# Kernel optimization log

Measured on AMD Instinct MI355X. Metric: run time of the kernel, lower is better.

Reference implementation:

```python
import jax, jax.numpy as jnp
from jax import lax
import numpy as np

INPUT = 80
H1 = 100
H2 = 50


def _lstm_layer(x, Wih, Whh, bih, bhh):
    """PyTorch-semantics single-layer LSTM, batch_first.
    x: [B,T,I]; Wih: [4H,I]; Whh: [4H,H]; biases: [4H]. Gate order: i,f,g,o.
    Returns full hidden sequence [B,T,H]."""
    B, T, _ = x.shape
    H = Whh.shape[1]
    # precompute input projections for all timesteps (one big GEMM)
    pre = jnp.einsum('bti,gi->tbg', x, Wih) + (bih + bhh)  # [T,B,4H]

    def step(carry, p):
        h, c = carry
        gates = p + h @ Whh.T  # [B,4H]
        i, f, g, o = jnp.split(gates, 4, axis=-1)
        i = jax.nn.sigmoid(i)
        f = jax.nn.sigmoid(f)
        g = jnp.tanh(g)
        o = jax.nn.sigmoid(o)
        c = f * c + i * g
        h = o * jnp.tanh(c)
        return (h, c), h

    h0 = jnp.zeros((B, H), x.dtype)
    (_, _), hs = lax.scan(step, (h0, h0), pre)  # hs: [T,B,H]
    return jnp.transpose(hs, (1, 0, 2))  # [B,T,H]


def setup_inputs() -> dict:
    key = jax.random.key(0)
    ks = jax.random.split(key, 9)
    B, T = 1024, 512
    s1 = 1.0 / np.sqrt(H1)
    s2 = 1.0 / np.sqrt(H2)
    return {
        'x': jax.random.normal(ks[0], (B, T, INPUT), dtype=jnp.float32),
        'Wih1': jax.random.uniform(ks[1], (4 * H1, INPUT), jnp.float32, -s1, s1),
        'Whh1': jax.random.uniform(ks[2], (4 * H1, H1), jnp.float32, -s1, s1),
        'bih1': jax.random.uniform(ks[3], (4 * H1,), jnp.float32, -s1, s1),
        'bhh1': jax.random.uniform(ks[4], (4 * H1,), jnp.float32, -s1, s1),
        'Wih2': jax.random.uniform(ks[5], (4 * H2, H1), jnp.float32, -s2, s2),
        'Whh2': jax.random.uniform(ks[6], (4 * H2, H2), jnp.float32, -s2, s2),
        'bih2': jax.random.uniform(ks[7], (4 * H2,), jnp.float32, -s2, s2),
        'bhh2': jax.random.uniform(ks[8], (4 * H2,), jnp.float32, -s2, s2),
    }


def reference(x, Wih1, Whh1, bih1, bhh1, Wih2, Whh2, bih2, bhh2):
    # Dropout layers are identity in eval mode.
    h1 = _lstm_layer(x, Wih1, Whh1, bih1, bhh1)   # [B,T,100]
    h2 = _lstm_layer(h1, Wih2, Whh2, bih2, bhh2)  # [B,T,50]
    return h2[:, -1, :]                            # [B,50]
```

## Files before the change

kernel.cpp:

```cpp
#include <hip/hip_runtime.h>

#define BT 1024
#define TT 512

__device__ __forceinline__ float sig_(float x) { return 1.f / (1.f + __expf(-x)); }
__device__ __forceinline__ float th_(float x)  { return 1.f - 2.f / (1.f + __expf(2.f * x)); }

template <int KS, int KPAD, int KH, int N, bool XMODE>
__device__ __forceinline__ void gp_stage(
    const float* __restrict__ A, const float* __restrict__ W,
    float (&As)[128][KPAD], float (&Bs)[KPAD][128],
    int tid, int n0, int by, int t0, int k0)
{
    constexpr int NQH = KH / 4;
#pragma unroll
    for (int ii = tid; ii < 128 * NQH; ii += 256) {
        int r = ii / NQH, q = ii % NQH;
        const float* src;
        if (XMODE) {
            int b  = (by & 7) * 128 + r;
            int tl = by >> 3;
            src = A + ((size_t)b * TT + (t0 + tl)) * KS;
        } else {
            src = A + (size_t)(by * 128 + r) * KS;
        }
        *(float4*)&As[r][q * 4] = *(const float4*)(src + k0 + q * 4);
    }
#pragma unroll
    for (int ii = tid; ii < 128 * NQH; ii += 256) {
        int n = ii & 127, kq = ii >> 7;
        float4 v = make_float4(0.f, 0.f, 0.f, 0.f);
        if (n0 + n < N) v = *(const float4*)(W + (size_t)(n0 + n) * KS + k0 + kq * 4);
        Bs[kq * 4 + 0][n] = v.x; Bs[kq * 4 + 1][n] = v.y;
        Bs[kq * 4 + 2][n] = v.z; Bs[kq * 4 + 3][n] = v.w;
    }
}

template <int KPAD, int KH>
__device__ __forceinline__ void gp_compute(
    const float (&As)[128][KPAD], const float (&Bs)[KPAD][128],
    float (&acc)[8][8], int tx, int ty)
{
    for (int kk = 0; kk < KH; kk += 4) {
        float4 bv[4][2];
#pragma unroll
        for (int r = 0; r < 4; r++) {
            bv[r][0] = *(const float4*)&Bs[kk + r][tx * 8];
            bv[r][1] = *(const float4*)&Bs[kk + r][tx * 8 + 4];
        }
#pragma unroll
        for (int i = 0; i < 8; i++) {
            float4 av = *(const float4*)&As[ty + 16 * i][kk];
#pragma unroll
            for (int s = 0; s < 2; s++) {
                acc[i][s*4+0] = fmaf(av.x, bv[0][s].x, acc[i][s*4+0]);
                acc[i][s*4+0] = fmaf(av.y, bv[1][s].x, acc[i][s*4+0]);
                acc[i][s*4+0] = fmaf(av.z, bv[2][s].x, acc[i][s*4+0]);
                acc[i][s*4+0] = fmaf(av.w, bv[3][s].x, acc[i][s*4+0]);
                acc[i][s*4+1] = fmaf(av.x, bv[0][s].y, acc[i][s*4+1]);
                acc[i][s*4+1] = fmaf(av.y, bv[1][s].y, acc[i][s*4+1]);
                acc[i][s*4+1] = fmaf(av.z, bv[2][s].y, acc[i][s*4+1]);
                acc[i][s*4+1] = fmaf(av.w, bv[3][s].y, acc[i][s*4+1]);
                acc[i][s*4+2] = fmaf(av.x, bv[0][s].z, acc[i][s*4+2]);
                acc[i][s*4+2] = fmaf(av.y, bv[1][s].z, acc[i][s*4+2]);
                acc[i][s*4+2] = fmaf(av.z, bv[2][s].z, acc[i][s*4+2]);
                acc[i][s*4+2] = fmaf(av.w, bv[3][s].z, acc[i][s*4+2]);
                acc[i][s*4+3] = fmaf(av.x, bv[0][s].w, acc[i][s*4+3]);
                acc[i][s*4+3] = fmaf(av.y, bv[1][s].w, acc[i][s*4+3]);
                acc[i][s*4+3] = fmaf(av.z, bv[2][s].w, acc[i][s*4+3]);
                acc[i][s*4+3] = fmaf(av.w, bv[3][s].w, acc[i][s*4+3]);
            }
        }
    }
}

template <int KS, int KPAD, int KH0, int N, bool XMODE>
__global__ __launch_bounds__(256, 3) void gemm_pre(
    const float* __restrict__ A, const float* __restrict__ W,
    const float* __restrict__ bih, const float* __restrict__ bhh,
    float* __restrict__ out, int t0)
{
    constexpr int KH1 = KS - KH0;
    __shared__ __align__(16) float As[128][KPAD];
    __shared__ __align__(16) float Bs[KPAD][128];
    const int tid = threadIdx.x;
    const int n0 = blockIdx.x * 128;
    const int by = blockIdx.y;
    const int Rbase = by * 128;
    const int tx = tid & 15, ty = tid >> 4;

    float acc[8][8];
#pragma unroll
    for (int i = 0; i < 8; i++)
#pragma unroll
        for (int j = 0; j < 8; j++) acc[i][j] = 0.f;

    gp_stage<KS, KPAD, KH0, N, XMODE>(A, W, As, Bs, tid, n0, by, t0, 0);
    __syncthreads();
    gp_compute<KPAD, KH0>(As, Bs, acc, tx, ty);
    __syncthreads();
    gp_stage<KS, KPAD, KH1, N, XMODE>(A, W, As, Bs, tid, n0, by, t0, KH0);
    __syncthreads();
    gp_compute<KPAD, KH1>(As, Bs, acc, tx, ty);

#pragma unroll
    for (int s = 0; s < 2; s++) {
        int n = n0 + tx * 8 + s * 4;
        if (n < N) {
            float4 bias;
            bias.x = bih[n] + bhh[n];         bias.y = bih[n + 1] + bhh[n + 1];
            bias.z = bih[n + 2] + bhh[n + 2]; bias.w = bih[n + 3] + bhh[n + 3];
#pragma unroll
            for (int i = 0; i < 8; i++) {
                size_t R = (size_t)Rbase + ty + 16 * i;
                float4 o;
                o.x = acc[i][s*4+0] + bias.x; o.y = acc[i][s*4+1] + bias.y;
                o.z = acc[i][s*4+2] + bias.z; o.w = acc[i][s*4+3] + bias.w;
                *(float4*)(out + R * N + n) = o;
            }
        }
    }
}

struct __align__(16) R1S {
    float hs[2][100];
    float pres[2][800];
    float gbuf[5 * 4 * 2 * 100];
};
struct __align__(16) R2S {
    float hs[2][50];
    float pres[2][400];
    float gbuf[5 * 4 * 2 * 50];
};
union __align__(16) FS { R1S r1; R2S r2[2]; };

__device__ __forceinline__ void rec1_body(
    R1S& s, int tid, int b0,
    const float* __restrict__ pre, const float* __restrict__ Whh,
    float* __restrict__ hseq, float* __restrict__ cst, int Tc, int first)
{
    const bool comp = tid < 500;
    const int j  = tid % 100;
    const int kq = tid / 100;

    float4 w[4][5];
    if (comp) {
#pragma unroll
        for (int g = 0; g < 4; g++) {
            const float4* W4 = (const float4*)(Whh + (size_t)(g * 100 + j) * 100);
#pragma unroll
            for (int q = 0; q < 5; q++) w[g][q] = W4[kq * 5 + q];
        }
    }

    const bool upd = tid < 200;
    const int ub = tid / 100, uj = tid % 100;
    float c = 0.f;
    if (upd) {
        float h = 0.f;
        if (!first) {
            h = hseq[((size_t)(Tc - 1) * BT + b0 + ub) * 100 + uj];
            c = cst[(size_t)(b0 + ub) * 100 + uj];
        }
        s.hs[ub][uj] = h;
        ((float4*)s.pres[0])[tid] = ((const float4*)(pre + (size_t)b0 * 400))[tid];
    }
    __syncthreads();

    int cur = 0;
    for (int t = 0; t < Tc; t++) {
        int tn = (t + 1 < Tc) ? (t + 1) : t;
        float4 pf0;
        if (upd)
            pf0 = ((const float4*)(pre + (size_t)tn * BT * 400 + (size_t)b0 * 400))[tid];

        if (comp) {
            float acc[4][2];
#pragma unroll
            for (int g = 0; g < 4; g++) { acc[g][0] = 0.f; acc[g][1] = 0.f; }
            const float4* h0 = (const float4*)s.hs[0];
            const float4* h1 = (const float4*)s.hs[1];
#pragma unroll
            for (int q = 0; q < 5; q++) {
                int f = kq * 5 + q;
                float4 v0 = h0[f], v1 = h1[f];
#pragma unroll
                for (int g = 0; g < 4; g++) {
                    float4 wq = w[g][q];
                    acc[g][0] = fmaf(wq.x, v0.x, acc[g][0]);
                    acc[g][0] = fmaf(wq.y, v0.y, acc[g][0]);
                    acc[g][0] = fmaf(wq.z, v0.z, acc[g][0]);
                    acc[g][0] = fmaf(wq.w, v0.w, acc[g][0]);
                    acc[g][1] = fmaf(wq.x, v1.x, acc[g][1]);
                    acc[g][1] = fmaf(wq.y, v1.y, acc[g][1]);
                    acc[g][1] = fmaf(wq.z, v1.z, acc[g][1]);
                    acc[g][1] = fmaf(wq.w, v1.w, acc[g][1]);
                }
            }
#pragma unroll
            for (int g = 0; g < 4; g++) {
                s.gbuf[((kq * 4 + g) * 2 + 0) * 100 + j] = acc[g][0];
                s.gbuf[((kq * 4 + g) * 2 + 1) * 100 + j] = acc[g][1];
            }
        }
        __syncthreads();

        if (upd) {
            const float* pb = s.pres[cur];
            float s0 = 0.f, s1 = 0.f, s2 = 0.f, s3 = 0.f;
#pragma unroll
            for (int q = 0; q < 5; q++) {
                int base = q * 800;
                s0 += s.gbuf[base + (0 * 2 + ub) * 100 + uj];
                s1 += s.gbuf[base + (1 * 2 + ub) * 100 + uj];
                s2 += s.gbuf[base + (2 * 2 + ub) * 100 + uj];
                s3 += s.gbuf[base + (3 * 2 + ub) * 100 + uj];
            }
            float xi = s0 + pb[ub * 400 + uj];
            float xf = s1 + pb[ub * 400 + 100 + uj];
            float xg = s2 + pb[ub * 400 + 200 + uj];
            float xo = s3 + pb[ub * 400 + 300 + uj];
            float ii = sig_(xi), ff = sig_(xf), gg = th_(xg), oo = sig_(xo);
            c = ff * c + ii * gg;
            float h = oo * th_(c);
            s.hs[ub][uj] = h;
            hseq[((size_t)t * BT + b0 + ub) * 100 + uj] = h;
            ((float4*)s.pres[cur ^ 1])[tid] = pf0;
        }
        __syncthreads();
        cur ^= 1;
    }
    if (upd) cst[(size_t)(b0 + ub) * 100 + uj] = c;
}

__device__ __forceinline__ void rec2_body(
    R2S& s, int tid, int b0,
    const float* __restrict__ pre2, const float* __restrict__ Whh,
    float* __restrict__ cst, float* __restrict__ hst, float* __restrict__ out,
    int Tc, int first)
{
    const bool comp = tid < 250;
    const int j  = tid % 50;
    const int kq = tid / 50;

    float2 w[4][5];
    if (comp) {
#pragma unroll
        for (int g = 0; g < 4; g++) {
            const float2* W2 = (const float2*)(Whh + (size_t)(g * 50 + j) * 50);
#pragma unroll
            for (int q = 0; q < 5; q++) w[g][q] = W2[kq * 5 + q];
        }
    }

    const bool upd = tid < 100;
    const int ub = tid / 50, uj = tid % 50;
    float c = 0.f, hlast = 0.f;
    if (upd) {
        float h = 0.f;
        if (!first) {
            h = hst[(size_t)(b0 + ub) * 50 + uj];
            c = cst[(size_t)(b0 + ub) * 50 + uj];
        }
        s.hs[ub][uj] = h;
        hlast = h;
        ((float4*)s.pres[0])[tid] = ((const float4*)(pre2 + (size_t)b0 * 200))[tid];
    }
    __syncthreads();

    int cur = 0;
    for (int t = 0; t < Tc; t++) {
        int tn = (t + 1 < Tc) ? (t + 1) : t;
        float4 pf0;
        if (upd)
            pf0 = ((const float4*)(pre2 + (size_t)tn * BT * 200 + (size_t)b0 * 200))[tid];

        if (comp) {
            float acc[4][2];
#pragma unroll
            for (int g = 0; g < 4; g++) { acc[g][0] = 0.f; acc[g][1] = 0.f; }
            const float2* hA = (const float2*)s.hs[0];
            const float2* hB = (const float2*)s.hs[1];
#pragma unroll
            for (int q = 0; q < 5; q++) {
                int f = kq * 5 + q;
                float2 v0 = hA[f], v1 = hB[f];
#pragma unroll
                for (int g = 0; g < 4; g++) {
                    float2 wq = w[g][q];
                    acc[g][0] = fmaf(wq.x, v0.x, acc[g][0]);
                    acc[g][0] = fmaf(wq.y, v0.y, acc[g][0]);
                    acc[g][1] = fmaf(wq.x, v1.x, acc[g][1]);
                    acc[g][1] = fmaf(wq.y, v1.y, acc[g][1]);
                }
            }
#pragma unroll
            for (int g = 0; g < 4; g++) {
                s.gbuf[((kq * 4 + g) * 2 + 0) * 50 + j] = acc[g][0];
                s.gbuf[((kq * 4 + g) * 2 + 1) * 50 + j] = acc[g][1];
            }
        }
        __syncthreads();

        if (upd) {
            const float* pb = s.pres[cur];
            float s0 = 0.f, s1 = 0.f, s2 = 0.f, s3 = 0.f;
#pragma unroll
            for (int q = 0; q < 5; q++) {
                int base = q * 400;
                s0 += s.gbuf[base + (0 * 2 + ub) * 50 + uj];
                s1 += s.gbuf[base + (1 * 2 + ub) * 50 + uj];
                s2 += s.gbuf[base + (2 * 2 + ub) * 50 + uj];
                s3 += s.gbuf[base + (3 * 2 + ub) * 50 + uj];
            }
            float xi = s0 + pb[ub * 200 + uj];
            float xf = s1 + pb[ub * 200 + 50 + uj];
            float xg = s2 + pb[ub * 200 + 100 + uj];
            float xo = s3 + pb[ub * 200 + 150 + uj];
            float ii = sig_(xi), ff = sig_(xf), gg = th_(xg), oo = sig_(xo);
            c = ff * c + ii * gg;
            float h = oo * th_(c);
            s.hs[ub][uj] = h;
            hlast = h;
            ((float4*)s.pres[cur ^ 1])[tid] = pf0;
        }
        __syncthreads();
        cur ^= 1;
    }
    if (upd) {
        cst[(size_t)(b0 + ub) * 50 + uj] = c;
        hst[(size_t)(b0 + ub) * 50 + uj] = hlast;
        out[(size_t)(b0 + ub) * 50 + uj] = hlast;
    }
}

__global__ __launch_bounds__(512, 4) void rec_fused(
    const float* __restrict__ pre1, const float* __restrict__ Whh1,
    float* __restrict__ h1seq, float* __restrict__ c1, int first1,
    const float* __restrict__ pre2, const float* __restrict__ Whh2,
    float* __restrict__ c2, float* __restrict__ h2st, float* __restrict__ out,
    int first2, int Tc)
{
    __shared__ FS sm;
    const int bx = blockIdx.x;
    const int tid = threadIdx.x;
    if (bx < 512) {
        rec1_body(sm.r1, tid, bx * 2, pre1, Whh1, h1seq, c1, Tc, first1);
    } else {
        const int h = tid >> 8;
        rec2_body(sm.r2[h], tid & 255, (bx - 512) * 4 + h * 2,
                  pre2, Whh2, c2, h2st, out, Tc, first2);
    }
}

__global__ __launch_bounds__(256, 4) void rec2k(
    const float* __restrict__ pre2, const float* __restrict__ Whh,
    float* __restrict__ cst, float* __restrict__ hst, float* __restrict__ out,
    int Tc, int first)
{
    __shared__ R2S s;
    rec2_body(s, threadIdx.x, blockIdx.x * 2, pre2, Whh, cst, hst, out, Tc, first);
}

extern "C" void kernel_launch(void* const* d_in, const int* in_sizes, int n_in,
                              void* d_out, int out_size, void* d_ws, size_t ws_size,
                              hipStream_t stream)
{
    const float* x    = (const float*)d_in[0];
    const float* Wih1 = (const float*)d_in[1];
    const float* Whh1 = (const float*)d_in[2];
    const float* bih1 = (const float*)d_in[3];
    const float* bhh1 = (const float*)d_in[4];
    const float* Wih2 = (const float*)d_in[5];
    const float* Whh2 = (const float*)d_in[6];
    const float* bih2 = (const float*)d_in[7];
    const float* bhh2 = (const float*)d_in[8];
    float* out = (float*)d_out;
    float* ws  = (float*)d_ws;

    int Tc = 64;
    auto need = [](int tc) -> size_t {
        return ((size_t)tc * 1024 * (400 + 100 + 200) +
                (size_t)1024 * 100 + (size_t)1024 * 50 * 2) * sizeof(float);
    };
    while (Tc > 1 && need(Tc) > ws_size) Tc >>= 1;

    float* pre1 = ws;
    float* h1s  = pre1 + (size_t)Tc * 1024 * 400;
    float* pre2 = h1s  + (size_t)Tc * 1024 * 100;
    float* c1   = pre2 + (size_t)Tc * 1024 * 200;
    float* c2   = c1 + 1024 * 100;
    float* h2st = c2 + 1024 * 50;

    const int nch = TT / Tc;

    gemm_pre<80, 40, 40, 400, true ><<<dim3(4, Tc * 8), 256, 0, stream>>>(
        x, Wih1, bih1, bhh1, pre1, 0);
    rec_fused<<<dim3(512), dim3(512), 0, stream>>>(
        pre1, Whh1, h1s, c1, 1, pre2, Whh2, c2, h2st, out, 0, Tc);

    for (int ch = 1; ch < nch; ch++) {
        int t0 = ch * Tc;
        gemm_pre<100, 52, 52, 200, false><<<dim3(2, Tc * 8), 256, 0, stream>>>(
            h1s, Wih2, bih2, bhh2, pre2, 0);
        gemm_pre<80, 40, 40, 400, true ><<<dim3(4, Tc * 8), 256, 0, stream>>>(
            x, Wih1, bih1, bhh1, pre1, t0);
        rec_fused<<<dim3(768), dim3(512), 0, stream>>>(
            pre1, Whh1, h1s, c1, 0,
            pre2, Whh2, c2, h2st, out, (ch == 1) ? 1 : 0, Tc);
    }

    gemm_pre<100, 52, 52, 200, false><<<dim3(2, Tc * 8), 256, 0, stream>>>(
        h1s, Wih2, bih2, bhh2, pre2, 0);
    rec2k<<<dim3(512), dim3(256), 0, stream>>>(
        pre2, Whh2, c2, h2st, out, Tc, 0);
}
```

Measured before the change: 2.458 ms.

## Fuse next-chunk layer-1 input GEMM into recurrent kernel with double-buffered pre1

Folds the layer-1 input-projection GEMM for the next time chunk into the fused recurrent kernel as extra blocks, writing into a second pre1 buffer. The aim is to overlap that GEMM with the latency-bound recurrence, which leaves the GPU underfilled, and to drop one launch per chunk. In exchange it doubles the pre1 workspace, which can force a smaller Tc. The GEMM blocks run at 512 threads with half of them idle, and they compete with the recurrence blocks for CUs and LDS.

```diff
diff --git a/kernel.cpp b/kernel.cpp
--- a/kernel.cpp
+++ b/kernel.cpp
@@ -75,17 +75,14 @@
 }
 
 template <int KS, int KPAD, int KH0, int N, bool XMODE>
-__global__ __launch_bounds__(256, 3) void gemm_pre(
+__device__ __forceinline__ void gemm_body(
+    float (&As)[128][KPAD], float (&Bs)[KPAD][128],
     const float* __restrict__ A, const float* __restrict__ W,
     const float* __restrict__ bih, const float* __restrict__ bhh,
-    float* __restrict__ out, int t0)
+    float* __restrict__ out, int t0, int tid, int bx, int by)
 {
     constexpr int KH1 = KS - KH0;
-    __shared__ __align__(16) float As[128][KPAD];
-    __shared__ __align__(16) float Bs[KPAD][128];
-    const int tid = threadIdx.x;
-    const int n0 = blockIdx.x * 128;
-    const int by = blockIdx.y;
+    const int n0 = bx * 128;
     const int Rbase = by * 128;
     const int tx = tid & 15, ty = tid >> 4;
 
@@ -120,6 +117,18 @@
             }
         }
     }
+}
+
+template <int KS, int KPAD, int KH0, int N, bool XMODE>
+__global__ __launch_bounds__(256, 3) void gemm_pre(
+    const float* __restrict__ A, const float* __restrict__ W,
+    const float* __restrict__ bih, const float* __restrict__ bhh,
+    float* __restrict__ out, int t0)
+{
+    __shared__ __align__(16) float As[128][KPAD];
+    __shared__ __align__(16) float Bs[KPAD][128];
+    gemm_body<KS, KPAD, KH0, N, XMODE>(As, Bs, A, W, bih, bhh, out, t0,
+                                       threadIdx.x, blockIdx.x, blockIdx.y);
 }
 
 struct __align__(16) R1S {
@@ -132,7 +141,8 @@
     float pres[2][400];
     float gbuf[5 * 4 * 2 * 50];
 };
-union __align__(16) FS { R1S r1; R2S r2[2]; };
+struct __align__(16) G1S { float As[128][40]; float Bs[40][128]; };
+union __align__(16) FS { R1S r1; R2S r2[2]; G1S g1; };
 
 __device__ __forceinline__ void rec1_body(
     R1S& s, int tid, int b0,
@@ -334,22 +344,30 @@
     }
 }
 
-__global__ __launch_bounds__(512, 4) void rec_fused(
-    const float* __restrict__ pre1, const float* __restrict__ Whh1,
+__global__ __launch_bounds__(512, 4) void rec_fused2(
+    const float* __restrict__ pre1r, const float* __restrict__ Whh1,
     float* __restrict__ h1seq, float* __restrict__ c1, int first1,
     const float* __restrict__ pre2, const float* __restrict__ Whh2,
     float* __restrict__ c2, float* __restrict__ h2st, float* __restrict__ out,
-    int first2, int Tc)
+    int first2, int has_r2,
+    const float* __restrict__ x, const float* __restrict__ Wih1,
+    const float* __restrict__ bih1, const float* __restrict__ bhh1,
+    float* __restrict__ pre1w, int t0n, int Tc)
 {
     __shared__ FS sm;
     const int bx = blockIdx.x;
     const int tid = threadIdx.x;
     if (bx < 512) {
-        rec1_body(sm.r1, tid, bx * 2, pre1, Whh1, h1seq, c1, Tc, first1);
-    } else {
+        rec1_body(sm.r1, tid, bx * 2, pre1r, Whh1, h1seq, c1, Tc, first1);
+    } else if (has_r2 && bx < 768) {
         const int h = tid >> 8;
         rec2_body(sm.r2[h], tid & 255, (bx - 512) * 4 + h * 2,
                   pre2, Whh2, c2, h2st, out, Tc, first2);
+    } else {
+        if (tid >= 256) return;
+        const int gid = bx - (has_r2 ? 768 : 512);
+        gemm_body<80, 40, 40, 400, true>(sm.g1.As, sm.g1.Bs,
+            x, Wih1, bih1, bhh1, pre1w, t0n, tid, gid & 3, gid >> 2);
     }
 }
 
@@ -380,34 +398,36 @@
 
     int Tc = 64;
     auto need = [](int tc) -> size_t {
-        return ((size_t)tc * 1024 * (400 + 100 + 200) +
+        return ((size_t)tc * 1024 * (400 * 2 + 100 + 200) +
                 (size_t)1024 * 100 + (size_t)1024 * 50 * 2) * sizeof(float);
     };
     while (Tc > 1 && need(Tc) > ws_size) Tc >>= 1;
 
-    float* pre1 = ws;
-    float* h1s  = pre1 + (size_t)Tc * 1024 * 400;
-    float* pre2 = h1s  + (size_t)Tc * 1024 * 100;
-    float* c1   = pre2 + (size_t)Tc * 1024 * 200;
-    float* c2   = c1 + 1024 * 100;
-    float* h2st = c2 + 1024 * 50;
+    float* pre1a = ws;
+    float* pre1b = pre1a + (size_t)Tc * 1024 * 400;
+    float* h1s   = pre1b + (size_t)Tc * 1024 * 400;
+    float* pre2  = h1s   + (size_t)Tc * 1024 * 100;
+    float* c1    = pre2  + (size_t)Tc * 1024 * 200;
+    float* c2    = c1 + 1024 * 100;
+    float* h2st  = c2 + 1024 * 50;
+    float* p1[2] = { pre1a, pre1b };
 
     const int nch = TT / Tc;
 
     gemm_pre<80, 40, 40, 400, true ><<<dim3(4, Tc * 8), 256, 0, stream>>>(
-        x, Wih1, bih1, bhh1, pre1, 0);
-    rec_fused<<<dim3(512), dim3(512), 0, stream>>>(
-        pre1, Whh1, h1s, c1, 1, pre2, Whh2, c2, h2st, out, 0, Tc);
-
-    for (int ch = 1; ch < nch; ch++) {
-        int t0 = ch * Tc;
-        gemm_pre<100, 52, 52, 200, false><<<dim3(2, Tc * 8), 256, 0, stream>>>(
-            h1s, Wih2, bih2, bhh2, pre2, 0);
-        gemm_pre<80, 40, 40, 400, true ><<<dim3(4, Tc * 8), 256, 0, stream>>>(
-            x, Wih1, bih1, bhh1, pre1, t0);
-        rec_fused<<<dim3(768), dim3(512), 0, stream>>>(
-            pre1, Whh1, h1s, c1, 0,
-            pre2, Whh2, c2, h2st, out, (ch == 1) ? 1 : 0, Tc);
+        x, Wih1, bih1, bhh1, p1[0], 0);
+
+    for (int ch = 0; ch < nch; ch++) {
+        if (ch >= 1)
+            gemm_pre<100, 52, 52, 200, false><<<dim3(2, Tc * 8), 256, 0, stream>>>(
+                h1s, Wih2, bih2, bhh2, pre2, 0);
+        int has_r2 = (ch >= 1) ? 1 : 0;
+        int has_g1 = (ch + 1 < nch) ? 1 : 0;
+        int nb = 512 + (has_r2 ? 256 : 0) + (has_g1 ? 2048 : 0);
+        rec_fused2<<<dim3(nb), dim3(512), 0, stream>>>(
+            p1[ch & 1], Whh1, h1s, c1, (ch == 0) ? 1 : 0,
+            pre2, Whh2, c2, h2st, out, (ch == 1) ? 1 : 0, has_r2,
+            x, Wih1, bih1, bhh1, p1[(ch + 1) & 1], (ch + 1) * Tc, Tc);
     }
 
     gemm_pre<100, 52, 52, 200, false><<<dim3(2, Tc * 8), 256, 0, stream>>>(
```

Result: no change. 2.430 ms (-1.2%).
